# Performance work log

Hardware: AMD Instinct MI355X
Metric: run time of the kernel (lower is better)

Reference implementation:

```python
import jax, jax.numpy as jnp
import numpy as np


def conv2d(x, w, dilation=1, padding=0):
    return jax.lax.conv_general_dilated(
        x, w, window_strides=(1, 1),
        padding=[(padding, padding), (padding, padding)],
        rhs_dilation=(dilation, dilation),
        dimension_numbers=('NCHW', 'OIHW', 'NCHW'))


def bn_relu(x, s, b):
    # inference-mode BatchNorm folded into per-channel scale/bias, then ReLU
    return jax.nn.relu(x * s[None, :, None, None] + b[None, :, None, None])


def resize_bilinear_ac(x, oh, ow):
    # bilinear interpolation with align_corners=True (matches F.interpolate)
    n, c, h, w = x.shape
    def axis_coords(o, i):
        if i == 1:
            z = jnp.zeros((o,), jnp.int32)
            return jnp.zeros((o,), x.dtype), z, z
        t = jnp.arange(o, dtype=x.dtype) * ((i - 1) / (o - 1))
        i0 = jnp.floor(t).astype(jnp.int32)
        i1 = jnp.minimum(i0 + 1, i - 1)
        return t - i0.astype(x.dtype), i0, i1
    fy, y0, y1 = axis_coords(oh, h)
    x = x[:, :, y0, :] * (1 - fy)[None, None, :, None] + x[:, :, y1, :] * fy[None, None, :, None]
    fx, x0, x1 = axis_coords(ow, w)
    x = x[:, :, :, x0] * (1 - fx) + x[:, :, :, x1] * fx
    return x


def unfold3x3_d2(x):
    # F.unfold(x, kernel_size=3, dilation=2, padding=2, stride=1) -> [n, c, 9, h*w]
    n, c, h, w = x.shape
    xp = jnp.pad(x, ((0, 0), (0, 0), (2, 2), (2, 2)))
    pats = [xp[:, :, i:i + h, j:j + w] for i in (0, 2, 4) for j in (0, 2, 4)]
    return jnp.stack(pats, axis=2).reshape(n, c, 9, h * w)


def setup_inputs() -> dict:
    key = jax.random.key(0)
    ks = iter(jax.random.split(key, 48))
    def rn(shape, scale=0.05):
        return jax.random.normal(next(ks), shape, jnp.float32) * scale
    d = {
        'c1': rn((1, 256, 64, 64), 1.0),
        'c2': rn((1, 512, 32, 32), 1.0),
        'x': rn((1, 4096, 32, 32), 1.0),
        'rf1_w': rn((64, 256, 3, 3)), 'rf1_s': jnp.ones((64,), jnp.float32), 'rf1_b': rn((64,)),
        'rf2_w': rn((64, 64, 3, 3)), 'rf2_s': jnp.ones((64,), jnp.float32), 'rf2_b': rn((64,)),
        'r2_w': rn((64, 512, 1, 1)), 'r2_s': jnp.ones((64,), jnp.float32), 'r2_b': rn((64,)),
        'a0_w': rn((512, 4096, 1, 1)), 'a0_s': jnp.ones((512,), jnp.float32), 'a0_b': rn((512,)),
        'a1_w': rn((512, 4096, 3, 3), 0.01), 'a1_s': jnp.ones((512,), jnp.float32), 'a1_b': rn((512,)),
        'a2_w': rn((512, 4096, 3, 3), 0.01), 'a2_s': jnp.ones((512,), jnp.float32), 'a2_b': rn((512,)),
        'a3_w': rn((512, 4096, 3, 3), 0.01), 'a3_s': jnp.ones((512,), jnp.float32), 'a3_b': rn((512,)),
        'a4_w': rn((512, 4096, 1, 1)), 'a4_s': jnp.ones((512,), jnp.float32), 'a4_b': rn((512,)),
        'ap_w': rn((512, 2560, 1, 1)), 'ap_s': jnp.ones((512,), jnp.float32), 'ap_b': rn((512,)),
        'c6_w': rn((19, 512, 1, 1)), 'c6_b': rn((19,)),
    }
    return d


def reference(c1, c2, x, rf1_w, rf1_s, rf1_b, rf2_w, rf2_s, rf2_b, r2_w, r2_s, r2_b,
              a0_w, a0_s, a0_b, a1_w, a1_s, a1_b, a2_w, a2_s, a2_b, a3_w, a3_s, a3_b,
              a4_w, a4_s, a4_b, ap_w, ap_s, ap_b, c6_w, c6_b):
    n, _, h, w = c1.shape
    # refine(c1): two 3x3 dilation-2 convs
    c1r = bn_relu(conv2d(c1, rf1_w, 2, 2), rf1_s, rf1_b)
    c1r = bn_relu(conv2d(c1r, rf2_w, 2, 2), rf2_s, rf2_b)  # [n,64,h,w]
    # refine2(interpolate(c2))
    c2r = bn_relu(conv2d(resize_bilinear_ac(c2, h, w), r2_w), r2_s, r2_b)  # [n,64,h,w]
    unf_c2 = unfold3x3_d2(c2r)  # [n,64,9,h*w]
    # energy[n,p,k] = sum_c c1r[n,c,p] * unf_c2[n,c,k,p]
    energy = jnp.einsum('ncp,nckp->npk', c1r.reshape(n, 64, h * w), unf_c2)
    att = jax.nn.softmax(energy, axis=-1)  # [n, h*w, 9]
    # ASPP on x (in=4096, out=512)
    f0 = bn_relu(conv2d(x, a0_w), a0_s, a0_b)
    f1 = bn_relu(conv2d(x, a1_w, 12, 12), a1_s, a1_b)
    f2 = bn_relu(conv2d(x, a2_w, 24, 24), a2_s, a2_b)
    f3 = bn_relu(conv2d(x, a3_w, 36, 36), a3_s, a3_b)
    gap = jnp.mean(x, axis=(2, 3), keepdims=True)
    f4 = resize_bilinear_ac(bn_relu(conv2d(gap, a4_w), a4_s, a4_b), x.shape[2], x.shape[3])
    out = bn_relu(conv2d(jnp.concatenate([f0, f1, f2, f3, f4], axis=1), ap_w), ap_s, ap_b)
    # local 3x3 window attention aggregation (dropout is eval-mode identity)
    unf_out = unfold3x3_d2(resize_bilinear_ac(out, h, w))  # [n,512,9,h*w]
    agg = jnp.einsum('npk,nckp->ncp', att, unf_out).reshape(n, 512, h, w)
    return conv2d(agg, c6_w) + c6_b[None, :, None, None]
```

## Files before the change

### kernel.cpp

```cpp
#include <hip/hip_runtime.h>
#include <hip/hip_bf16.h>


typedef unsigned short u16;
typedef short bf16x8 __attribute__((ext_vector_type(8)));
typedef float f32x4  __attribute__((ext_vector_type(4)));
typedef u16   u16x8  __attribute__((ext_vector_type(8)));

__device__ __forceinline__ float bf2f(u16 u) {
    return __uint_as_float(((unsigned int)u) << 16);
}
__device__ __forceinline__ u16 f2bf(float f) {
    unsigned u = __float_as_uint(f);
    return (u16)((u + 0x7FFFu + ((u >> 16) & 1u)) >> 16);
}
__device__ __forceinline__ float loadv(const void* p, long i, int f32) {
    return f32 ? ((const float*)p)[i] : bf2f(((const u16*)p)[i]);
}
__device__ __forceinline__ u16 loadbf(const void* p, long i, int f32) {
    return f32 ? f2bf(((const float*)p)[i]) : ((const u16*)p)[i];
}

__device__ __forceinline__ void gload16(const u16* g, u16* l) {
    __builtin_amdgcn_global_load_lds(
        (const __attribute__((address_space(1))) unsigned int*)(g),
        (__attribute__((address_space(3))) unsigned int*)(l), 16, 0, 0);
}

__global__ __launch_bounds__(256) void detect_kernel(
    const u16* __restrict__ c1, int* __restrict__ flag)
{
    __shared__ int cnt;
    if (threadIdx.x == 0) cnt = 0;
    __syncthreads();
    int local = 0;
    for (int i = threadIdx.x; i < 16384; i += 256) {
        u16 u = c1[i];
        if ((u & 0x7F80) >= 0x4F00) local++;
    }
    atomicAdd(&cnt, local);
    __syncthreads();
    if (threadIdx.x == 0) flag[0] = (cnt > 256) ? 1 : 0;
}

__global__ __launch_bounds__(256) void zero_kernel(float* __restrict__ p, int n)
{
    for (int g = blockIdx.x * 256 + threadIdx.x; g < n; g += gridDim.x * 256)
        p[g] = 0.f;
}


__global__ __launch_bounds__(256) void xpose_bn(
    const void* __restrict__ src, u16* __restrict__ dst,
    const void* __restrict__ s, const void* __restrict__ b,
    const int* __restrict__ flag, int flagged, int dobn, int C, int P,
    int dstC, int coff)
{
    __shared__ u16 T[64][72];
    const int fl = flag[0];
    const int srcf32 = flagged ? fl : 1;
    const int p0 = blockIdx.x * 64, c0 = blockIdx.y * 64;
    const int t = threadIdx.x;
    {
        int c = t >> 2, pq = (t & 3) * 16;
        float sc = 1.f, bc = 0.f;
        if (dobn) { sc = loadv(s, c0 + c, fl); bc = loadv(b, c0 + c, fl); }
        const long sb = (long)(c0 + c) * P + p0 + pq;
        if (srcf32) {
            const float* sp = (const float*)src + sb;
#pragma unroll
            for (int i = 0; i < 16; i += 4) {
                float4 v = *(const float4*)(sp + i);
                float vv[4] = {v.x, v.y, v.z, v.w};
#pragma unroll
                for (int j = 0; j < 4; j++) {
                    float u = vv[j];
                    if (dobn) u = fmaxf(u * sc + bc, 0.f);
                    T[pq + i + j][c] = f2bf(u);
                }
            }
        } else {
            const u16* sp = (const u16*)src + sb;
#pragma unroll
            for (int i = 0; i < 16; i++) T[pq + i][c] = sp[i];
        }
    }
    __syncthreads();
    {
        int p = t >> 2, cq = (t & 3) * 16;
        u16x8 v0, v1;
#pragma unroll
        for (int i = 0; i < 8; i++) { v0[i] = T[p][cq + i]; v1[i] = T[p][cq + 8 + i]; }
        *(u16x8*)&dst[(long)(p0 + p) * dstC + coff + c0 + cq] = v0;
        *(u16x8*)&dst[(long)(p0 + p) * dstC + coff + c0 + cq + 8] = v1;
    }
}

__global__ __launch_bounds__(256) void xform_w9(
    const void* __restrict__ w, u16* __restrict__ W9, const int* __restrict__ flag,
    int O, int C)
{
    const int f32 = flag[0];
    const int o = blockIdx.y;
    const int c = blockIdx.x * 256 + threadIdx.x;
    if (c >= C) return;
    const long src = ((long)o * C + c) * 9;
    u16 v[9];
    if (f32) {
        const float* p = (const float*)w + src;
#pragma unroll
        for (int j = 0; j < 9; j++) v[j] = f2bf(p[j]);
    } else {
        const u16* p = (const u16*)w + src;
#pragma unroll
        for (int j = 0; j < 9; j++) v[j] = p[j];
    }
#pragma unroll
    for (int j = 0; j < 9; j++)
        W9[(long)j * O * C + (long)o * C + c] = v[j];
}

__global__ __launch_bounds__(256) void xform_w1(
    const void* __restrict__ w, u16* __restrict__ Wo, const int* __restrict__ flag,
    int ldi, int off, int st, int logC)
{
    const int f32 = flag[0];
    long g = (long)blockIdx.x * 256 + threadIdx.x;
    long o = g >> logC;
    int c = (int)(g & ((1 << logC) - 1));
    Wo[g] = loadbf(w, o * ldi + off + (long)c * st, f32);
}

template<int MF>
__global__ __launch_bounds__(256, 4) void conv_gemm(
    const u16* __restrict__ W2, const u16* __restrict__ X2,
    const u16* __restrict__ zpage, float* __restrict__ OUT,
    int K, int O, int taps, int d, int logIW, int P,
    int nbo, int nbp, int kcs, int swz)
{
    __shared__ __align__(16) u16 Ws[4][MF * 2048];
    __shared__ __align__(16) u16 Xs[4][4096];

    const int tid = threadIdx.x;
    int bo, bp, bz;
    {
        int pid = blockIdx.x;
        if (swz) {
            int xcd = pid & 7, j = pid >> 3;
            bp = j % nbp;
            int g = j / nbp;
            int G = xcd + 8 * g;
            bo = G % nbo; bz = G / nbo;
        } else {
            bp = pid % nbp;
            int q = pid / nbp;
            bo = q % nbo; bz = q / nbo;
        }
    }
    const int kb = bz * kcs;
    const int IW = 1 << logIW;

    const int wave = tid >> 6, lane = tid & 63;
    const int quad = lane >> 4, l15 = lane & 15;

    int mask = 1;
    if (taps == 9) {
        const int rb = 128 >> logIW;
        const int ty0 = bp * rb;
        mask = 0;
        for (int t = 0; t < 9; t++) {
            int dy = (t / 3 - 1) * d;
            if (ty0 + rb - 1 + dy >= 0 && ty0 + dy < IW) mask |= (1 << t);
        }
    }
    const int nIt = (kcs >> 5) * __popc(mask);

    int wrow[MF], wk[MF];
#pragma unroll
    for (int li = 0; li < MF; li++) {
        int bb = li * 4096 + tid * 16;
        int l = bb ^ (((bb >> 7) & 3) << 4);
        wrow[li] = l >> 6; wk[li] = ((l >> 4) & 3) * 8;
    }
    int xrow[2], xk[2];
#pragma unroll
    for (int li = 0; li < 2; li++) {
        int bb = li * 4096 + tid * 16;
        int l = bb ^ (((bb >> 7) & 3) << 4);
        xrow[li] = l >> 6; xk[li] = ((l >> 4) & 3) * 8;
    }

    const long wplane = (long)O * K;

    f32x4 acc[MF][8];
#pragma unroll
    for (int mi = 0; mi < MF; mi++)
#pragma unroll
        for (int j = 0; j < 8; j++) {
            f32x4 z = {0.f, 0.f, 0.f, 0.f};
            acc[mi][j] = z;
        }

    int arow[MF];
#pragma unroll
    for (int mi = 0; mi < MF; mi++) {
        int ao = (wave * (MF * 16) + mi * 16 + l15) * 64 + quad * 16;
        arow[mi] = ao ^ (((ao >> 7) & 3) << 4);
    }

    int tt = __ffs(mask) - 1;
    int kc = kb;

    auto STAGE = [&](int buf) {
        int dy = 0, dx = 0;
        if (taps == 9) { dy = (tt / 3 - 1) * d; dx = (tt % 3 - 1) * d; }
#pragma unroll
        for (int li = 0; li < MF; li++)
            gload16(W2 + (long)tt * wplane + (long)(bo * (MF * 64) + wrow[li]) * K + kc + wk[li],
                    &Ws[buf][li * 2048 + tid * 8]);
#pragma unroll
        for (int li = 0; li < 2; li++) {
            int pg = bp * 128 + xrow[li];
            const u16* src;
            if (taps == 9) {
                int yy = (pg >> logIW) + dy, xx = (pg & (IW - 1)) + dx;
                src = ((unsigned)yy < (unsigned)IW && (unsigned)xx < (unsigned)IW)
                    ? X2 + (long)((yy << logIW) | xx) * K + kc + xk[li] : zpage;
            } else {
                src = X2 + (long)pg * K + kc + xk[li];
            }
            gload16(src, &Xs[buf][li * 2048 + tid * 8]);
        }
        int rem = mask >> (tt + 1);
        if (rem) tt += __ffs(rem);
        else { tt = __ffs(mask) - 1; kc += 32; }
    };

    STAGE(0);
    if (nIt > 1) STAGE(1);
    if (nIt > 2) STAGE(2);

    for (int i = 0; i < nIt; i++) {
        const int ex = nIt - 1 - i;
        if constexpr (MF == 2) {
            if (ex >= 3)      asm volatile("s_waitcnt vmcnt(12)" ::: "memory");
            else if (ex == 2) asm volatile("s_waitcnt vmcnt(8)" ::: "memory");
            else if (ex == 1) asm volatile("s_waitcnt vmcnt(4)" ::: "memory");
            else              asm volatile("s_waitcnt vmcnt(0)" ::: "memory");
        } else {
            if (ex >= 3)      asm volatile("s_waitcnt vmcnt(9)" ::: "memory");
            else if (ex == 2) asm volatile("s_waitcnt vmcnt(6)" ::: "memory");
            else if (ex == 1) asm volatile("s_waitcnt vmcnt(3)" ::: "memory");
            else              asm volatile("s_waitcnt vmcnt(0)" ::: "memory");
        }
        __builtin_amdgcn_s_barrier();
        __builtin_amdgcn_sched_barrier(0);

        const int cur = i & 3;
        bf16x8 a[MF];
#pragma unroll
        for (int mi = 0; mi < MF; mi++)
            a[mi] = *(const bf16x8*)&Ws[cur][arow[mi] >> 1];
#pragma unroll
        for (int j = 0; j < 8; j++) {
            int boff = (j * 16 + l15) * 64 + quad * 16;
            boff ^= ((boff >> 7) & 3) << 4;
            bf16x8 b = *(const bf16x8*)&Xs[cur][boff >> 1];
#pragma unroll
            for (int mi = 0; mi < MF; mi++)
                acc[mi][j] = __builtin_amdgcn_mfma_f32_16x16x32_bf16(a[mi], b, acc[mi][j], 0, 0, 0);
        }
        if (i + 3 < nIt) STAGE((i + 3) & 3);
    }

#pragma unroll
    for (int mi = 0; mi < MF; mi++)
#pragma unroll
        for (int j = 0; j < 8; j++) {
            int pgl = bp * 128 + j * 16 + l15;
            long ob = (long)(bo * (MF * 64) + wave * (MF * 16) + mi * 16 + quad * 4);
#pragma unroll
            for (int r = 0; r < 4; r++)
                atomicAdd(&OUT[(ob + r) * P + pgl], acc[mi][j][r]);
        }
}

__global__ __launch_bounds__(256) void conv_mfma(
    const void* __restrict__ W, const void* __restrict__ X, float* __restrict__ OUT,
    const int* __restrict__ flag, int x_ext,
    int K, int wrow, int wstride, int woff, int taps, int d, int logIW)
{
    __shared__ __align__(16) u16 Ws[64 * 40];
    __shared__ __align__(16) u16 Xs[128 * 40];

    const int IW = 1 << logIW;
    const int NP = IW * IW;
    const int wf32 = flag[0];
    const int xf32 = x_ext ? wf32 : 1;

    const int tid = threadIdx.x;
    const int bo = blockIdx.x, bp = blockIdx.y;
    const int kcs = K / gridDim.z;
    const int kb = blockIdx.z * kcs;

    const int w_o = tid >> 2, w_kg = (tid & 3) * 8;
    const int x_p = tid >> 1, x_kg = (tid & 1) * 16;
    const int pg  = bp * 128 + x_p;
    const int py  = pg >> logIW, px = pg & (IW - 1);
    const int ty0 = (bp * 128) >> logIW;
    const int ty1 = ty0 + (128 >> logIW) - 1;

    const int wave = tid >> 6, lane = tid & 63;
    const int quad = lane >> 4, l15 = lane & 15;

    f32x4 acc[8];
#pragma unroll
    for (int j = 0; j < 8; j++) {
        f32x4 z = {0.f, 0.f, 0.f, 0.f};
        acc[j] = z;
    }

    const long wbase_o = (long)(bo * 64 + w_o) * wrow + woff;

    for (int kc = kb; kc < kb + kcs; kc += 32) {
        for (int t = 0; t < taps; t++) {
            int dy = 0, dx = 0, wt = 0;
            if (taps == 9) { dy = (t / 3 - 1) * d; dx = (t % 3 - 1) * d; wt = t; }
            if (ty1 + dy < 0 || ty0 + dy >= IW) continue;

            {
                u16 tv[8];
                if (wstride == 1) {
                    long idx = wbase_o + kc + w_kg;
                    if (wf32) {
                        float4 v0 = *(const float4*)((const float*)W + idx);
                        float4 v1 = *(const float4*)((const float*)W + idx + 4);
                        tv[0] = f2bf(v0.x); tv[1] = f2bf(v0.y);
                        tv[2] = f2bf(v0.z); tv[3] = f2bf(v0.w);
                        tv[4] = f2bf(v1.x); tv[5] = f2bf(v1.y);
                        tv[6] = f2bf(v1.z); tv[7] = f2bf(v1.w);
                    } else {
                        ushort4 v0 = *(const ushort4*)((const u16*)W + idx);
                        ushort4 v1 = *(const ushort4*)((const u16*)W + idx + 4);
                        tv[0] = v0.x; tv[1] = v0.y; tv[2] = v0.z; tv[3] = v0.w;
                        tv[4] = v1.x; tv[5] = v1.y; tv[6] = v1.z; tv[7] = v1.w;
                    }
                } else {
                    long idx = wbase_o + wt + (long)(kc + w_kg) * 9;
#pragma unroll
                    for (int i = 0; i < 8; i++)
                        tv[i] = loadbf(W, idx + (long)i * 9, wf32);
                }
                *(ushort4*)&Ws[w_o * 40 + w_kg]     = make_ushort4(tv[0], tv[1], tv[2], tv[3]);
                *(ushort4*)&Ws[w_o * 40 + w_kg + 4] = make_ushort4(tv[4], tv[5], tv[6], tv[7]);
            }
            {
                int yy = py + dy, xv = px + dx;
                bool ok = ((unsigned)yy < (unsigned)IW) && ((unsigned)xv < (unsigned)IW);
                u16 tv[16];
                if (ok) {
                    long idx = (long)(kc + x_kg) * NP + yy * IW + xv;
                    if (xf32) {
#pragma unroll
                        for (int i = 0; i < 16; i++)
                            tv[i] = f2bf(((const float*)X)[idx + (long)i * NP]);
                    } else {
#pragma unroll
                        for (int i = 0; i < 16; i++)
                            tv[i] = ((const u16*)X)[idx + (long)i * NP];
                    }
                } else {
#pragma unroll
                    for (int i = 0; i < 16; i++) tv[i] = 0;
                }
                *(ushort4*)&Xs[x_p * 40 + x_kg]      = make_ushort4(tv[0], tv[1], tv[2], tv[3]);
                *(ushort4*)&Xs[x_p * 40 + x_kg + 4]  = make_ushort4(tv[4], tv[5], tv[6], tv[7]);
                *(ushort4*)&Xs[x_p * 40 + x_kg + 8]  = make_ushort4(tv[8], tv[9], tv[10], tv[11]);
                *(ushort4*)&Xs[x_p * 40 + x_kg + 12] = make_ushort4(tv[12], tv[13], tv[14], tv[15]);
            }
            __syncthreads();
            {
                bf16x8 a = *(const bf16x8*)&Ws[(wave * 16 + l15) * 40 + quad * 8];
#pragma unroll
                for (int j = 0; j < 8; j++) {
                    bf16x8 b = *(const bf16x8*)&Xs[(j * 16 + l15) * 40 + quad * 8];
                    acc[j] = __builtin_amdgcn_mfma_f32_16x16x32_bf16(a, b, acc[j], 0, 0, 0);
                }
            }
            __syncthreads();
        }
    }

#pragma unroll
    for (int j = 0; j < 8; j++) {
        int pgl = bp * 128 + j * 16 + l15;
        long ob = (long)(bo * 64 + wave * 16 + quad * 4);
#pragma unroll
        for (int r = 0; r < 4; r++)
            atomicAdd(&OUT[(ob + r) * NP + pgl], acc[j][r]);
    }
}

__global__ __launch_bounds__(256) void ep_bnrelu(
    float* __restrict__ buf, const void* __restrict__ s, const void* __restrict__ b,
    const int* __restrict__ flag, int logN, int total)
{
    int f32 = flag[0];
    int g = blockIdx.x * 256 + threadIdx.x;
    if (g >= total) return;
    int c = g >> logN;
    float v = buf[g] * loadv(s, c, f32) + loadv(b, c, f32);
    buf[g] = fmaxf(v, 0.f);
}

__global__ __launch_bounds__(256) void ep_aspp(
    float* __restrict__ buf, const float* __restrict__ f4con,
    const void* __restrict__ s, const void* __restrict__ b, const int* __restrict__ flag)
{
    int f32 = flag[0];
    int g = blockIdx.x * 256 + threadIdx.x;
    int c = g >> 10;
    float v = (buf[g] + f4con[c]) * loadv(s, c, f32) + loadv(b, c, f32);
    buf[g] = fmaxf(v, 0.f);
}

__global__ __launch_bounds__(256) void resize_bn(
    const float* __restrict__ in, float* __restrict__ out,
    const void* __restrict__ s, const void* __restrict__ b,
    const int* __restrict__ flag, int dobn)
{
    int g = blockIdx.x * 256 + threadIdx.x;
    int c = g >> 12, p = g & 4095;
    int oy = p >> 6, ox = p & 63;
    const float r = 31.0f / 63.0f;
    float tyf = oy * r, txf = ox * r;
    int y0 = (int)tyf, x0 = (int)txf;
    float fy = tyf - y0, fx = txf - x0;
    int y1 = y0 + 1 > 31 ? 31 : y0 + 1;
    int x1 = x0 + 1 > 31 ? 31 : x0 + 1;
    const float* pc = in + c * 1024;
    float v00 = pc[y0 * 32 + x0], v01 = pc[y0 * 32 + x1];
    float v10 = pc[y1 * 32 + x0], v11 = pc[y1 * 32 + x1];
    float v = (1.f - fy) * ((1.f - fx) * v00 + fx * v01) +
              fy * ((1.f - fx) * v10 + fx * v11);
    if (dobn) v = fmaxf(v * loadv(s, c, flag[0]) + loadv(b, c, flag[0]), 0.f);
    out[g] = v;
}

__global__ __launch_bounds__(256) void attn_kernel(
    const float* __restrict__ c1r, const float* __restrict__ c2r, float* __restrict__ att)
{
    int tid = threadIdx.x;
    int p = blockIdx.x * 4 + (tid >> 6);
    int lane = tid & 63;
    int y = p >> 6, x = p & 63;
    float a = c1r[lane * 4096 + p];
    float e[9];
#pragma unroll
    for (int ky = 0; ky < 3; ky++)
#pragma unroll
        for (int kx = 0; kx < 3; kx++) {
            int yy = y + 2 * (ky - 1), xx = x + 2 * (kx - 1);
            float v = 0.f;
            if (yy >= 0 && yy < 64 && xx >= 0 && xx < 64)
                v = a * c2r[lane * 4096 + yy * 64 + xx];
#pragma unroll
            for (int off = 32; off; off >>= 1) v += __shfl_xor(v, off);
            e[ky * 3 + kx] = v;
        }
    float m = e[0];
#pragma unroll
    for (int k = 1; k < 9; k++) m = fmaxf(m, e[k]);
    float ssum = 0.f;
#pragma unroll
    for (int k = 0; k < 9; k++) ssum += __expf(e[k] - m);
    if (lane < 9) {
        float mye = e[0];
#pragma unroll
        for (int k = 1; k < 9; k++)
            if (lane == k) mye = e[k];
        att[p * 9 + lane] = __expf(mye - m) / ssum;
    }
}

__global__ __launch_bounds__(256) void gap_kernel(
    const void* __restrict__ x, const int* __restrict__ flag, float* __restrict__ gap)
{
    int f32 = flag[0];
    int tid = threadIdx.x;
    int c = blockIdx.x * 4 + (tid >> 6);
    int lane = tid & 63;
    long base = (long)c * 1024;
    float ssum = 0.f;
#pragma unroll
    for (int i = 0; i < 16; i++) ssum += loadv(x, base + lane + i * 64, f32);
#pragma unroll
    for (int off = 32; off; off >>= 1) ssum += __shfl_xor(ssum, off);
    if (lane == 0) gap[c] = ssum * (1.0f / 1024.0f);
}

__global__ __launch_bounds__(256) void f4_kernel(
    const void* __restrict__ w, const float* __restrict__ gap,
    const void* __restrict__ s, const void* __restrict__ b,
    const int* __restrict__ flag, float* __restrict__ f4c)
{
    int f32 = flag[0];
    int tid = threadIdx.x;
    int o = blockIdx.x * 4 + (tid >> 6);
    int lane = tid & 63;
    long base = (long)o * 4096;
    float ssum = 0.f;
#pragma unroll
    for (int i = 0; i < 64; i++)
        ssum += loadv(w, base + lane + i * 64, f32) * gap[lane + i * 64];
#pragma unroll
    for (int off = 32; off; off >>= 1) ssum += __shfl_xor(ssum, off);
    if (lane == 0) f4c[o] = fmaxf(ssum * loadv(s, o, f32) + loadv(b, o, f32), 0.f);
}

__global__ __launch_bounds__(256) void f4con_kernel(
    const void* __restrict__ ap_w, const float* __restrict__ f4c,
    const int* __restrict__ flag, float* __restrict__ f4con)
{
    int f32 = flag[0];
    int tid = threadIdx.x;
    int o = blockIdx.x * 4 + (tid >> 6);
    int lane = tid & 63;
    long base = (long)o * 2560 + 2048;
    float ssum = 0.f;
#pragma unroll
    for (int i = 0; i < 8; i++)
        ssum += loadv(ap_w, base + lane + i * 64, f32) * f4c[lane + i * 64];
#pragma unroll
    for (int off = 32; off; off >>= 1) ssum += __shfl_xor(ssum, off);
    if (lane == 0) f4con[o] = ssum;
}

__global__ __launch_bounds__(256) void vs_kernel(
    const float* __restrict__ aspp, const void* __restrict__ w,
    const int* __restrict__ flag, float* __restrict__ Vs)
{
    int f32 = flag[0];
    int p = blockIdx.x * 256 + threadIdx.x;
    int q = blockIdx.y;
    long wb = (long)q * 512;
    float a0 = 0.f, a1 = 0.f, a2 = 0.f, a3 = 0.f;
    for (int c = 0; c < 512; c += 4) {
        a0 = fmaf(loadv(w, wb + c + 0, f32), aspp[(c + 0) * 1024 + p], a0);
        a1 = fmaf(loadv(w, wb + c + 1, f32), aspp[(c + 1) * 1024 + p], a1);
        a2 = fmaf(loadv(w, wb + c + 2, f32), aspp[(c + 2) * 1024 + p], a2);
        a3 = fmaf(loadv(w, wb + c + 3, f32), aspp[(c + 3) * 1024 + p], a3);
    }
    Vs[q * 1024 + p] = (a0 + a1) + (a2 + a3);
}

__global__ __launch_bounds__(256) void final_kernel(
    const float* __restrict__ att, const float* __restrict__ V,
    const void* __restrict__ bias, const int* __restrict__ flag, void* __restrict__ out)
{
    int f32 = flag[0];
    int g = blockIdx.x * 256 + threadIdx.x;
    int q = g >> 12, p = g & 4095;
    int y = p >> 6, x = p & 63;
    const float* a = att + p * 9;
    const float* v = V + q * 4096;
    float acc = loadv(bias, q, f32);
#pragma unroll
    for (int ky = 0; ky < 3; ky++)
#pragma unroll
        for (int kx = 0; kx < 3; kx++) {
            int yy = y + 2 * (ky - 1), xx = x + 2 * (kx - 1);
            if (yy >= 0 && yy < 64 && xx >= 0 && xx < 64)
                acc += a[ky * 3 + kx] * v[yy * 64 + xx];
        }
    if (f32) ((float*)out)[g] = acc;
    else     ((__hip_bfloat16*)out)[g] = __float2bfloat16(acc);
}

extern "C" void kernel_launch(void* const* d_in, const int* in_sizes, int n_in,
                              void* d_out, int out_size, void* d_ws, size_t ws_size,
                              hipStream_t stream)
{
    const void* c1    = d_in[0];
    const void* c2    = d_in[1];
    const void* x     = d_in[2];
    const void* rf1_w = d_in[3];
    const void* rf1_s = d_in[4];
    const void* rf1_b = d_in[5];
    const void* rf2_w = d_in[6];
    const void* rf2_s = d_in[7];
    const void* rf2_b = d_in[8];
    const void* r2_w  = d_in[9];
    const void* r2_s  = d_in[10];
    const void* r2_b  = d_in[11];
    const void* a0_w  = d_in[12];
    const void* a0_s  = d_in[13];
    const void* a0_b  = d_in[14];
    const void* a1_w  = d_in[15];
    const void* a1_s  = d_in[16];
    const void* a1_b  = d_in[17];
    const void* a2_w  = d_in[18];
    const void* a2_s  = d_in[19];
    const void* a2_b  = d_in[20];
    const void* a3_w  = d_in[21];
    const void* a3_s  = d_in[22];
    const void* a3_b  = d_in[23];
    const void* a4_w  = d_in[24];
    const void* a4_s  = d_in[25];
    const void* a4_b  = d_in[26];
    const void* ap_w  = d_in[27];
    const void* ap_s  = d_in[28];
    const void* ap_b  = d_in[29];
    const void* c6_w  = d_in[30];
    const void* c6_b  = d_in[31];

    const long F_BUFR = 0;
    const long F_C1R  = 262144;
    const long F_BUFC = 524288;
    const long F_ASPP = 589824;
    const long F_ZP   = 1114112;
    const long F_TMP  = 1114368;
    const long F_C2R  = 1638656;
    const long F_ATT  = 1900800;
    const long F_GAPV = 1937664;
    const long F_F4C  = 1941760;
    const long F_F4CO = 1942272;
    const long F_VS   = 1942784;
    const long F_V    = 1962240;
    const long F_FLAG = 2040064;
    const long F_X2   = 2040128;
    const long F_W2   = 4137280;
    const long F_W1   = 13574464;
    const long F_END  = 14623040;

    float* ws    = (float*)d_ws;
    float* bufR  = ws + F_BUFR;
    float* c1r   = ws + F_C1R;
    float* bufC  = ws + F_BUFC;
    float* aspp  = ws + F_ASPP;
    float* tmp   = ws + F_TMP;
    float* c2r   = ws + F_C2R;
    float* att   = ws + F_ATT;
    float* gapv  = ws + F_GAPV;
    float* f4c   = ws + F_F4C;
    float* f4con = ws + F_F4CO;
    float* Vs    = ws + F_VS;
    float* V     = ws + F_V;
    int*   flag  = (int*)(ws + F_FLAG);
    u16*   X2u   = (u16*)(ws + F_X2);
    u16*   W2u   = (u16*)(ws + F_W2);
    u16*   T2all = (u16*)(ws + F_W1);
    const u16* zp16 = (const u16*)(ws + F_ZP);

    u16* X1u   = W2u;
    u16* W9Ru  = W2u + 1048576;
    u16* X1Bu  = W2u + 1196032;
    u16* W9R2u = W2u + 1458176;
    u16* X1Cu  = W2u + 1495040;
    u16* W1Ru  = W2u + 2019328;
    u16* a0Wu  = W2u;
    u16* a3Wu  = W2u + 2097152;
    u16* WAPu  = W2u + 4194304;

    const bool big = ws_size >= (size_t)F_END * 4;

    detect_kernel<<<1, 256, 0, stream>>>((const u16*)c1, flag);
    zero_kernel<<<1024, 256, 0, stream>>>(ws, 1114368);

    if (big) {
        xpose_bn<<<dim3(64, 4), 256, 0, stream>>>(c1, X1u, nullptr, nullptr,
                                                  flag, 1, 0, 256, 4096, 256, 0);
        xform_w9<<<dim3(1, 64), 256, 0, stream>>>(rf1_w, W9Ru, flag, 64, 256);
        conv_gemm<1><<<256, 256, 0, stream>>>(W9Ru, X1u, zp16, bufR,
                                              256, 64, 9, 2, 6, 4096, 1, 32, 32, 1);
        xpose_bn<<<dim3(64, 1), 256, 0, stream>>>(bufR, X1Bu, rf1_s, rf1_b,
                                                  flag, 0, 1, 64, 4096, 64, 0);
        xform_w9<<<dim3(1, 64), 256, 0, stream>>>(rf2_w, W9R2u, flag, 64, 64);
        conv_gemm<1><<<64, 256, 0, stream>>>(W9R2u, X1Bu, zp16, c1r,
                                             64, 64, 9, 2, 6, 4096, 1, 32, 32, 0);
        ep_bnrelu<<<1024, 256, 0, stream>>>(c1r, rf2_s, rf2_b, flag, 12, 262144);

        xpose_bn<<<dim3(16, 8), 256, 0, stream>>>(c2, X1Cu, nullptr, nullptr,
                                                  flag, 1, 0, 512, 1024, 512, 0);
        xform_w1<<<128, 256, 0, stream>>>(r2_w, W1Ru, flag, 512, 0, 1, 9);
        conv_gemm<1><<<32, 256, 0, stream>>>(W1Ru, X1Cu, zp16, bufC,
                                             512, 64, 1, 0, 5, 1024, 1, 8, 128, 0);
        resize_bn<<<1024, 256, 0, stream>>>(bufC, c2r, r2_s, r2_b, flag, 1);

        attn_kernel<<<1024, 256, 0, stream>>>(c1r, c2r, att);

        gap_kernel<<<1024, 256, 0, stream>>>(x, flag, gapv);
        f4_kernel<<<128, 256, 0, stream>>>(a4_w, gapv, a4_s, a4_b, flag, f4c);
        f4con_kernel<<<128, 256, 0, stream>>>(ap_w, f4c, flag, f4con);

        xpose_bn<<<dim3(16, 64), 256, 0, stream>>>(x, X2u, nullptr, nullptr,
                                                   flag, 1, 0, 4096, 1024, 4096, 0);

        zero_kernel<<<512, 256, 0, stream>>>(tmp, 524288);
        xform_w1<<<8192, 256, 0, stream>>>(a0_w, a0Wu, flag, 4096, 0, 1, 12);
        conv_gemm<2><<<256, 256, 0, stream>>>(a0Wu, X2u, zp16, tmp,
                                              4096, 512, 1, 0, 5, 1024, 4, 8, 512, 1);
        xpose_bn<<<dim3(16, 8), 256, 0, stream>>>(tmp, T2all, a0_s, a0_b,
                                                  flag, 0, 1, 512, 1024, 2048, 0);
        zero_kernel<<<512, 256, 0, stream>>>(tmp, 524288);
        xform_w9<<<dim3(16, 512), 256, 0, stream>>>(a1_w, W2u, flag, 512, 4096);
        conv_gemm<2><<<512, 256, 0, stream>>>(W2u, X2u, zp16, tmp,
                                              4096, 512, 9, 12, 5, 1024, 4, 8, 256, 1);
        xpose_bn<<<dim3(16, 8), 256, 0, stream>>>(tmp, T2all, a1_s, a1_b,
                                                  flag, 0, 1, 512, 1024, 2048, 512);
        zero_kernel<<<512, 256, 0, stream>>>(tmp, 524288);
        xform_w9<<<dim3(16, 512), 256, 0, stream>>>(a2_w, W2u, flag, 512, 4096);
        conv_gemm<2><<<512, 256, 0, stream>>>(W2u, X2u, zp16, tmp,
                                              4096, 512, 9, 24, 5, 1024, 4, 8, 256, 1);
        xpose_bn<<<dim3(16, 8), 256, 0, stream>>>(tmp, T2all, a2_s, a2_b,
                                                  flag, 0, 1, 512, 1024, 2048, 1024);
        zero_kernel<<<512, 256, 0, stream>>>(tmp, 524288);
        xform_w1<<<8192, 256, 0, stream>>>(a3_w, a3Wu, flag, 36864, 4, 9, 12);
        conv_gemm<2><<<256, 256, 0, stream>>>(a3Wu, X2u, zp16, tmp,
                                              4096, 512, 1, 0, 5, 1024, 4, 8, 512, 1);
        xpose_bn<<<dim3(16, 8), 256, 0, stream>>>(tmp, T2all, a3_s, a3_b,
                                                  flag, 0, 1, 512, 1024, 2048, 1536);
        xform_w1<<<4096, 256, 0, stream>>>(ap_w, WAPu, flag, 2560, 0, 1, 11);
        conv_gemm<2><<<256, 256, 0, stream>>>(WAPu, T2all, zp16, aspp,
                                              2048, 512, 1, 0, 5, 1024, 4, 8, 256, 1);
        ep_aspp<<<2048, 256, 0, stream>>>(aspp, f4con, ap_s, ap_b, flag);
    } else {
        conv_mfma<<<dim3(1, 32, 4), 256, 0, stream>>>(rf1_w, c1, bufR, flag, 1,
                                                      256, 256 * 9, 9, 0, 9, 2, 6);
        ep_bnrelu<<<1024, 256, 0, stream>>>(bufR, rf1_s, rf1_b, flag, 12, 262144);
        conv_mfma<<<dim3(1, 32, 2), 256, 0, stream>>>(rf2_w, bufR, c1r, flag, 0,
                                                      64, 64 * 9, 9, 0, 9, 2, 6);
        ep_bnrelu<<<1024, 256, 0, stream>>>(c1r, rf2_s, rf2_b, flag, 12, 262144);
        conv_mfma<<<dim3(1, 8, 4), 256, 0, stream>>>(r2_w, c2, bufC, flag, 1,
                                                     512, 512, 1, 0, 1, 0, 5);
        resize_bn<<<1024, 256, 0, stream>>>(bufC, c2r, r2_s, r2_b, flag, 1);
        attn_kernel<<<1024, 256, 0, stream>>>(c1r, c2r, att);
        gap_kernel<<<1024, 256, 0, stream>>>(x, flag, gapv);
        f4_kernel<<<128, 256, 0, stream>>>(a4_w, gapv, a4_s, a4_b, flag, f4c);
        f4con_kernel<<<128, 256, 0, stream>>>(ap_w, f4c, flag, f4con);

        zero_kernel<<<512, 256, 0, stream>>>(tmp, 524288);
        conv_mfma<<<dim3(8, 8, 4), 256, 0, stream>>>(a0_w, x, tmp, flag, 1,
                                                     4096, 4096, 1, 0, 1, 0, 5);
        ep_bnrelu<<<2048, 256, 0, stream>>>(tmp, a0_s, a0_b, flag, 10, 524288);
        conv_mfma<<<dim3(8, 8, 2), 256, 0, stream>>>(ap_w, tmp, aspp, flag, 0,
                                                     512, 2560, 1, 0, 1, 0, 5);
        zero_kernel<<<512, 256, 0, stream>>>(tmp, 524288);
        conv_mfma<<<dim3(8, 8, 8), 256, 0, stream>>>(a1_w, x, tmp, flag, 1,
                                                     4096, 4096 * 9, 9, 0, 9, 12, 5);
        ep_bnrelu<<<2048, 256, 0, stream>>>(tmp, a1_s, a1_b, flag, 10, 524288);
        conv_mfma<<<dim3(8, 8, 2), 256, 0, stream>>>(ap_w, tmp, aspp, flag, 0,
                                                     512, 2560, 1, 512, 1, 0, 5);
        zero_kernel<<<512, 256, 0, stream>>>(tmp, 524288);
        conv_mfma<<<dim3(8, 8, 8), 256, 0, stream>>>(a2_w, x, tmp, flag, 1,
                                                     4096, 4096 * 9, 9, 0, 9, 24, 5);
        ep_bnrelu<<<2048, 256, 0, stream>>>(tmp, a2_s, a2_b, flag, 10, 524288);
        conv_mfma<<<dim3(8, 8, 2), 256, 0, stream>>>(ap_w, tmp, aspp, flag, 0,
                                                     512, 2560, 1, 1024, 1, 0, 5);
        zero_kernel<<<512, 256, 0, stream>>>(tmp, 524288);
        conv_mfma<<<dim3(8, 8, 4), 256, 0, stream>>>(a3_w, x, tmp, flag, 1,
                                                     4096, 4096 * 9, 9, 4, 1, 0, 5);
        ep_bnrelu<<<2048, 256, 0, stream>>>(tmp, a3_s, a3_b, flag, 10, 524288);
        conv_mfma<<<dim3(8, 8, 2), 256, 0, stream>>>(ap_w, tmp, aspp, flag, 0,
                                                     512, 2560, 1, 1536, 1, 0, 5);
        ep_aspp<<<2048, 256, 0, stream>>>(aspp, f4con, ap_s, ap_b, flag);
    }

    vs_kernel<<<dim3(4, 19), 256, 0, stream>>>(aspp, c6_w, flag, Vs);
    resize_bn<<<304, 256, 0, stream>>>(Vs, V, nullptr, nullptr, flag, 0);
    final_kernel<<<304, 256, 0, stream>>>(att, V, c6_b, flag, d_out);
}
```

Measured before the change: 673.4 us.

## Store GEMM operands in K-slab-blocked layout and use triple-buffered pipeline

Weights and activations are now written in a [K/32][rows][32] blocked layout, so each 32-wide K chunk of a tile is one contiguous region instead of rows strided by the full K. The conv_gemm loader addresses are rewritten for this layout to improve DRAM/L2 locality of the async LDS loads. The shared-memory ring shrinks from four stages to three, which cuts LDS use and may raise occupancy but gives less prefetch depth. MFMA issue is also wrapped in s_setprio.

Result: no change. 670.6 us (-0.4%).

```diff
diff --git a/kernel.cpp b/kernel.cpp
--- a/kernel.cpp
+++ b/kernel.cpp
@@ -53,8 +53,7 @@
 __global__ __launch_bounds__(256) void xpose_bn(
     const void* __restrict__ src, u16* __restrict__ dst,
     const void* __restrict__ s, const void* __restrict__ b,
-    const int* __restrict__ flag, int flagged, int dobn, int C, int P,
-    int dstC, int coff)
+    const int* __restrict__ flag, int flagged, int dobn, int C, int P, int coff)
 {
     __shared__ u16 T[64][72];
     const int fl = flag[0];
@@ -91,8 +90,10 @@
         u16x8 v0, v1;
 #pragma unroll
         for (int i = 0; i < 8; i++) { v0[i] = T[p][cq + i]; v1[i] = T[p][cq + 8 + i]; }
-        *(u16x8*)&dst[(long)(p0 + p) * dstC + coff + c0 + cq] = v0;
-        *(u16x8*)&dst[(long)(p0 + p) * dstC + coff + c0 + cq + 8] = v1;
+        const int cabs = coff + c0 + cq;
+        const long base = ((long)(cabs >> 5) * P + (p0 + p)) * 32 + (cabs & 31);
+        *(u16x8*)&dst[base] = v0;
+        *(u16x8*)&dst[base + 8] = v1;
     }
 }
 
@@ -115,20 +116,22 @@
 #pragma unroll
         for (int j = 0; j < 9; j++) v[j] = p[j];
     }
+    const int C32 = C >> 5;
 #pragma unroll
     for (int j = 0; j < 9; j++)
-        W9[(long)j * O * C + (long)o * C + c] = v[j];
+        W9[((long)(j * C32 + (c >> 5)) * O + o) * 32 + (c & 31)] = v[j];
 }
 
 __global__ __launch_bounds__(256) void xform_w1(
     const void* __restrict__ w, u16* __restrict__ Wo, const int* __restrict__ flag,
-    int ldi, int off, int st, int logC)
+    int ldi, int off, int st, int logC, int O)
 {
     const int f32 = flag[0];
     long g = (long)blockIdx.x * 256 + threadIdx.x;
     long o = g >> logC;
     int c = (int)(g & ((1 << logC) - 1));
-    Wo[g] = loadbf(w, o * ldi + off + (long)c * st, f32);
+    u16 v = loadbf(w, o * ldi + off + (long)c * st, f32);
+    Wo[((long)(c >> 5) * O + o) * 32 + (c & 31)] = v;
 }
 
 template<int MF>
@@ -138,8 +141,8 @@
     int K, int O, int taps, int d, int logIW, int P,
     int nbo, int nbp, int kcs, int swz)
 {
-    __shared__ __align__(16) u16 Ws[4][MF * 2048];
-    __shared__ __align__(16) u16 Xs[4][4096];
+    __shared__ __align__(16) u16 Ws[3][MF * 2048];
+    __shared__ __align__(16) u16 Xs[3][4096];
 
     const int tid = threadIdx.x;
     int bo, bp, bz;
@@ -175,22 +178,22 @@
     }
     const int nIt = (kcs >> 5) * __popc(mask);
 
-    int wrow[MF], wk[MF];
+    int lW[MF];
 #pragma unroll
     for (int li = 0; li < MF; li++) {
         int bb = li * 4096 + tid * 16;
-        int l = bb ^ (((bb >> 7) & 3) << 4);
-        wrow[li] = l >> 6; wk[li] = ((l >> 4) & 3) * 8;
-    }
-    int xrow[2], xk[2];
+        lW[li] = bb ^ (((bb >> 7) & 3) << 4);
+    }
+    int xr[2], xoff[2];
 #pragma unroll
     for (int li = 0; li < 2; li++) {
         int bb = li * 4096 + tid * 16;
         int l = bb ^ (((bb >> 7) & 3) << 4);
-        xrow[li] = l >> 6; xk[li] = ((l >> 4) & 3) * 8;
-    }
-
-    const long wplane = (long)O * K;
+        xr[li] = l >> 6;
+        xoff[li] = (l & 63) >> 1;
+    }
+
+    const int K32 = K >> 5;
 
     f32x4 acc[MF][8];
 #pragma unroll
@@ -214,20 +217,21 @@
     auto STAGE = [&](int buf) {
         int dy = 0, dx = 0;
         if (taps == 9) { dy = (tt / 3 - 1) * d; dx = (tt % 3 - 1) * d; }
+        const long wb = ((long)(tt * K32 + (kc >> 5)) * O + bo * (MF * 64)) * 32;
 #pragma unroll
         for (int li = 0; li < MF; li++)
-            gload16(W2 + (long)tt * wplane + (long)(bo * (MF * 64) + wrow[li]) * K + kc + wk[li],
-                    &Ws[buf][li * 2048 + tid * 8]);
+            gload16(W2 + wb + (lW[li] >> 1), &Ws[buf][li * 2048 + tid * 8]);
+        const long xslab = (long)(kc >> 5) * P * 32;
 #pragma unroll
         for (int li = 0; li < 2; li++) {
-            int pg = bp * 128 + xrow[li];
+            int pg = bp * 128 + xr[li];
             const u16* src;
             if (taps == 9) {
                 int yy = (pg >> logIW) + dy, xx = (pg & (IW - 1)) + dx;
                 src = ((unsigned)yy < (unsigned)IW && (unsigned)xx < (unsigned)IW)
-                    ? X2 + (long)((yy << logIW) | xx) * K + kc + xk[li] : zpage;
+                    ? X2 + xslab + (long)((yy << logIW) + xx) * 32 + xoff[li] : zpage;
             } else {
-                src = X2 + (long)pg * K + kc + xk[li];
+                src = X2 + xslab + (long)pg * 32 + xoff[li];
             }
             gload16(src, &Xs[buf][li * 2048 + tid * 8]);
         }
@@ -238,29 +242,25 @@
 
     STAGE(0);
     if (nIt > 1) STAGE(1);
-    if (nIt > 2) STAGE(2);
 
     for (int i = 0; i < nIt; i++) {
         const int ex = nIt - 1 - i;
         if constexpr (MF == 2) {
-            if (ex >= 3)      asm volatile("s_waitcnt vmcnt(12)" ::: "memory");
-            else if (ex == 2) asm volatile("s_waitcnt vmcnt(8)" ::: "memory");
-            else if (ex == 1) asm volatile("s_waitcnt vmcnt(4)" ::: "memory");
-            else              asm volatile("s_waitcnt vmcnt(0)" ::: "memory");
+            if (ex >= 1) asm volatile("s_waitcnt vmcnt(4)" ::: "memory");
+            else         asm volatile("s_waitcnt vmcnt(0)" ::: "memory");
         } else {
-            if (ex >= 3)      asm volatile("s_waitcnt vmcnt(9)" ::: "memory");
-            else if (ex == 2) asm volatile("s_waitcnt vmcnt(6)" ::: "memory");
-            else if (ex == 1) asm volatile("s_waitcnt vmcnt(3)" ::: "memory");
-            else              asm volatile("s_waitcnt vmcnt(0)" ::: "memory");
+            if (ex >= 1) asm volatile("s_waitcnt vmcnt(3)" ::: "memory");
+            else         asm volatile("s_waitcnt vmcnt(0)" ::: "memory");
         }
         __builtin_amdgcn_s_barrier();
         __builtin_amdgcn_sched_barrier(0);
 
-        const int cur = i & 3;
+        const int cur = i % 3;
         bf16x8 a[MF];
 #pragma unroll
         for (int mi = 0; mi < MF; mi++)
             a[mi] = *(const bf16x8*)&Ws[cur][arow[mi] >> 1];
+        __builtin_amdgcn_s_setprio(1);
 #pragma unroll
         for (int j = 0; j < 8; j++) {
             int boff = (j * 16 + l15) * 64 + quad * 16;
@@ -270,7 +270,8 @@
             for (int mi = 0; mi < MF; mi++)
                 acc[mi][j] = __builtin_amdgcn_mfma_f32_16x16x32_bf16(a[mi], b, acc[mi][j], 0, 0, 0);
         }
-        if (i + 3 < nIt) STAGE((i + 3) & 3);
+        __builtin_amdgcn_s_setprio(0);
+        if (i + 2 < nIt) STAGE((i + 2) % 3);
     }
 
 #pragma unroll
@@ -669,20 +670,20 @@
 
     if (big) {
         xpose_bn<<<dim3(64, 4), 256, 0, stream>>>(c1, X1u, nullptr, nullptr,
-                                                  flag, 1, 0, 256, 4096, 256, 0);
+                                                  flag, 1, 0, 256, 4096, 0);
         xform_w9<<<dim3(1, 64), 256, 0, stream>>>(rf1_w, W9Ru, flag, 64, 256);
         conv_gemm<1><<<256, 256, 0, stream>>>(W9Ru, X1u, zp16, bufR,
                                               256, 64, 9, 2, 6, 4096, 1, 32, 32, 1);
         xpose_bn<<<dim3(64, 1), 256, 0, stream>>>(bufR, X1Bu, rf1_s, rf1_b,
-                                                  flag, 0, 1, 64, 4096, 64, 0);
+                                                  flag, 0, 1, 64, 4096, 0);
         xform_w9<<<dim3(1, 64), 256, 0, stream>>>(rf2_w, W9R2u, flag, 64, 64);
         conv_gemm<1><<<64, 256, 0, stream>>>(W9R2u, X1Bu, zp16, c1r,
                                              64, 64, 9, 2, 6, 4096, 1, 32, 32, 0);
         ep_bnrelu<<<1024, 256, 0, stream>>>(c1r, rf2_s, rf2_b, flag, 12, 262144);
 
         xpose_bn<<<dim3(16, 8), 256, 0, stream>>>(c2, X1Cu, nullptr, nullptr,
-                                                  flag, 1, 0, 512, 1024, 512, 0);
-        xform_w1<<<128, 256, 0, stream>>>(r2_w, W1Ru, flag, 512, 0, 1, 9);
+                                                  flag, 1, 0, 512, 1024, 0);
+        xform_w1<<<128, 256, 0, stream>>>(r2_w, W1Ru, flag, 512, 0, 1, 9, 64);
         conv_gemm<1><<<32, 256, 0, stream>>>(W1Ru, X1Cu, zp16, bufC,
                                              512, 64, 1, 0, 5, 1024, 1, 8, 128, 0);
         resize_bn<<<1024, 256, 0, stream>>>(bufC, c2r, r2_s, r2_b, flag, 1);
@@ -694,33 +695,33 @@
         f4con_kernel<<<128, 256, 0, stream>>>(ap_w, f4c, flag, f4con);
 
         xpose_bn<<<dim3(16, 64), 256, 0, stream>>>(x, X2u, nullptr, nullptr,
-                                                   flag, 1, 0, 4096, 1024, 4096, 0);
+                                                   flag, 1, 0, 4096, 1024, 0);
 
         zero_kernel<<<512, 256, 0, stream>>>(tmp, 524288);
-        xform_w1<<<8192, 256, 0, stream>>>(a0_w, a0Wu, flag, 4096, 0, 1, 12);
+        xform_w1<<<8192, 256, 0, stream>>>(a0_w, a0Wu, flag, 4096, 0, 1, 12, 512);
         conv_gemm<2><<<256, 256, 0, stream>>>(a0Wu, X2u, zp16, tmp,
                                               4096, 512, 1, 0, 5, 1024, 4, 8, 512, 1);
         xpose_bn<<<dim3(16, 8), 256, 0, stream>>>(tmp, T2all, a0_s, a0_b,
-                                                  flag, 0, 1, 512, 1024, 2048, 0);
+                                                  flag, 0, 1, 512, 1024, 0);
         zero_kernel<<<512, 256, 0, stream>>>(tmp, 524288);
         xform_w9<<<dim3(16, 512), 256, 0, stream>>>(a1_w, W2u, flag, 512, 4096);
         conv_gemm<2><<<512, 256, 0, stream>>>(W2u, X2u, zp16, tmp,
                                               4096, 512, 9, 12, 5, 1024, 4, 8, 256, 1);
         xpose_bn<<<dim3(16, 8), 256, 0, stream>>>(tmp, T2all, a1_s, a1_b,
-                                                  flag, 0, 1, 512, 1024, 2048, 512);
+                                                  flag, 0, 1, 512, 1024, 512);
         zero_kernel<<<512, 256, 0, stream>>>(tmp, 524288);
         xform_w9<<<dim3(16, 512), 256, 0, stream>>>(a2_w, W2u, flag, 512, 4096);
         conv_gemm<2><<<512, 256, 0, stream>>>(W2u, X2u, zp16, tmp,
                                               4096, 512, 9, 24, 5, 1024, 4, 8, 256, 1);
         xpose_bn<<<dim3(16, 8), 256, 0, stream>>>(tmp, T2all, a2_s, a2_b,
-                                                  flag, 0, 1, 512, 1024, 2048, 1024);
+                                                  flag, 0, 1, 512, 1024, 1024);
         zero_kernel<<<512, 256, 0, stream>>>(tmp, 524288);
-        xform_w1<<<8192, 256, 0, stream>>>(a3_w, a3Wu, flag, 36864, 4, 9, 12);
+        xform_w1<<<8192, 256, 0, stream>>>(a3_w, a3Wu, flag, 36864, 4, 9, 12, 512);
         conv_gemm<2><<<256, 256, 0, stream>>>(a3Wu, X2u, zp16, tmp,
                                               4096, 512, 1, 0, 5, 1024, 4, 8, 512, 1);
         xpose_bn<<<dim3(16, 8), 256, 0, stream>>>(tmp, T2all, a3_s, a3_b,
-                                                  flag, 0, 1, 512, 1024, 2048, 1536);
-        xform_w1<<<4096, 256, 0, stream>>>(ap_w, WAPu, flag, 2560, 0, 1, 11);
+                                                  flag, 0, 1, 512, 1024, 1536);
+        xform_w1<<<4096, 256, 0, stream>>>(ap_w, WAPu, flag, 2560, 0, 1, 11, 512);
         conv_gemm<2><<<256, 256, 0, stream>>>(WAPu, T2all, zp16, aspp,
                                               2048, 512, 1, 0, 5, 1024, 4, 8, 256, 1);
         ep_aspp<<<2048, 256, 0, stream>>>(aspp, f4con, ap_s, ap_b, flag);
```
